# Kernel tuning notes

Hardware: AMD Instinct MI355X
Metric: run time of the kernel (lower is better)

Reference implementation:

```python
import jax, jax.numpy as jnp
import numpy as np
import math

B, S, D, H = 2, 2048, 1024, 16
HD = D // H  # head dim = 64


def setup_inputs() -> dict:
    key = jax.random.key(0)
    ks = jax.random.split(key, 8)
    scale = 1.0 / math.sqrt(D)
    return {
        "x": jax.random.normal(ks[0], (B, S, D), dtype=jnp.float32),
        "mask": jax.random.randint(ks[1], (B, S, S), 0, 2).astype(bool),
        "Wq": jax.random.normal(ks[2], (D, D), dtype=jnp.float32) * scale,
        "bq": jax.random.normal(ks[3], (D,), dtype=jnp.float32) * 0.01,
        "Wk": jax.random.normal(ks[4], (D, D), dtype=jnp.float32) * scale,
        "bk": jax.random.normal(ks[5], (D,), dtype=jnp.float32) * 0.01,
        "Wv": jax.random.normal(ks[6], (D, D), dtype=jnp.float32) * scale,
        "bv": jax.random.normal(ks[7], (D,), dtype=jnp.float32) * 0.01,
    }


def reference(x, mask, Wq, bq, Wk, bk, Wv, bv):
    # Linear projections (weights stored as [in, out])
    q = x @ Wq + bq  # [B,S,D]
    k = x @ Wk + bk
    v = x @ Wv + bv
    # split heads -> [B,H,S,HD]
    q = q.reshape(B, S, H, HD).transpose(0, 2, 1, 3)
    k = k.reshape(B, S, H, HD).transpose(0, 2, 1, 3)
    v = v.reshape(B, S, H, HD).transpose(0, 2, 1, 3)
    scores = jnp.einsum("bhqd,bhkd->bhqk", q, k) / jnp.sqrt(jnp.float32(HD))
    # Faithful to the source: masked_fill_(mask, -inf) is immediately
    # overwritten by masked_fill_(mask, 0), so masked positions end up 0
    # BEFORE the softmax (a quirk of the original module).
    scores = jnp.where(mask[:, None, :, :], 0.0, scores)
    attn = jax.nn.softmax(scores, axis=-1)  # dropout=0.0 (eval)
    out = jnp.einsum("bhqk,bhkd->bhqd", attn, v)
    return out.transpose(0, 2, 1, 3).reshape(B, S, D)
```

## Files before the change

kernel.cpp:

```cpp
#include <hip/hip_runtime.h>
#include <hip/hip_bf16.h>
#include <cstdint>
#include <cstddef>

static constexpr int B_ = 2, S_ = 2048, D_ = 1024, H_ = 16, HD_ = 64;

typedef float f32x4 __attribute__((ext_vector_type(4)));
typedef short bf16x8 __attribute__((ext_vector_type(8)));

__device__ __forceinline__ unsigned short f2bf(float f) {
    union { float f; unsigned int u; } v; v.f = f;
    unsigned int r = v.u + 0x7FFFu + ((v.u >> 16) & 1u);
    return (unsigned short)(r >> 16);
}

__device__ __forceinline__ unsigned pack2bf(float a, float b) {
#if __has_builtin(__builtin_amdgcn_cvt_pk_bf16_f32)
    auto p = __builtin_amdgcn_cvt_pk_bf16_f32(a, b);
    unsigned u; __builtin_memcpy(&u, &p, 4);
    return u;
#else
    return (unsigned)f2bf(a) | ((unsigned)f2bf(b) << 16);
#endif
}

__global__ __launch_bounds__(256)
void cast_x(const float* __restrict__ x, unsigned short* __restrict__ o) {
    size_t i = ((size_t)blockIdx.x * 256 + threadIdx.x) * 8;
    float4 a = *(const float4*)(x + i);
    float4 c = *(const float4*)(x + i + 4);
    uint4 r;
    r.x = pack2bf(a.x, a.y);
    r.y = pack2bf(a.z, a.w);
    r.z = pack2bf(c.x, c.y);
    r.w = pack2bf(c.z, c.w);
    *(uint4*)(o + i) = r;
}

__global__ __launch_bounds__(256)
void mask_pack(const int* __restrict__ m, unsigned char* __restrict__ o) {
    size_t i = ((size_t)blockIdx.x * 256 + threadIdx.x) * 16;
    uint4 r;
    unsigned w[4];
    #pragma unroll
    for (int g = 0; g < 4; ++g) {
        int4 v = *(const int4*)(m + i + g * 4);
        w[g] = (v.x ? 1u : 0u) | (v.y ? 1u << 8 : 0u) |
               (v.z ? 1u << 16 : 0u) | (v.w ? 1u << 24 : 0u);
    }
    r.x = w[0]; r.y = w[1]; r.z = w[2]; r.w = w[3];
    *(uint4*)(o + i) = r;
}

__global__ __launch_bounds__(256)
void transpose_w(const float* __restrict__ Wq, const float* __restrict__ Wk,
                 const float* __restrict__ Wv, unsigned short* __restrict__ wt) {
    const int mat = blockIdx.z;
    const float* __restrict__ W = (mat == 0) ? Wq : (mat == 1) ? Wk : Wv;
    unsigned short* __restrict__ o = wt + (size_t)mat * D_ * D_;
    const int n0 = blockIdx.x * 64, k0 = blockIdx.y * 64;
    __shared__ unsigned short Ts[64][72];
    const int t = threadIdx.x;
    {
        const int nl = t & 63, kb = t >> 6;
        #pragma unroll
        for (int i = 0; i < 16; ++i) {
            int k = kb + i * 4;
            Ts[nl][k] = f2bf(W[(size_t)(k0 + k) * D_ + n0 + nl]);
        }
    }
    __syncthreads();
    {
        const int kl = t & 63, nb = t >> 6;
        #pragma unroll
        for (int i = 0; i < 16; ++i) {
            int n = nb + i * 4;
            o[(size_t)(n0 + n) * D_ + k0 + kl] = Ts[n][kl];
        }
    }
}

__global__ __launch_bounds__(256)
void qkv_gemm(const unsigned short* __restrict__ xb, const unsigned short* __restrict__ wt,
              const float* __restrict__ bq, const float* __restrict__ bk,
              const float* __restrict__ bv,
              unsigned short* __restrict__ qo, unsigned short* __restrict__ ko,
              unsigned short* __restrict__ vto) {
    const int bx = blockIdx.x;
    const int by = blockIdx.y;
    const int mat = bx >> 3;
    const int ncol0 = (bx & 7) * 128;
    const float* __restrict__ bias = (mat == 0) ? bq : (mat == 1) ? bk : bv;
    const unsigned short* __restrict__ Wm = wt + (size_t)mat * D_ * D_;

    __shared__ unsigned short As[128][40];
    __shared__ unsigned short Bs[128][40];

    const int t = threadIdx.x;
    const int w = t >> 6, lane = t & 63;
    const int l15 = lane & 15, quad = lane >> 4;
    const int mw = (w >> 1) * 64, nw = (w & 1) * 64;
    const int rowBase = by * 128;

    f32x4 acc[4][4] = {};

    for (int kt = 0; kt < D_; kt += 32) {
        __syncthreads();
        #pragma unroll
        for (int i = 0; i < 2; ++i) {
            int c = t + i * 256;
            int r = c >> 2, q = c & 3;
            *(uint4*)&As[r][q * 8] =
                *(const uint4*)(xb + (size_t)(rowBase + r) * D_ + kt + q * 8);
            *(uint4*)&Bs[r][q * 8] =
                *(const uint4*)(Wm + (size_t)(ncol0 + r) * D_ + kt + q * 8);
        }
        __syncthreads();

        bf16x8 a[4], b[4];
        #pragma unroll
        for (int i = 0; i < 4; ++i)
            a[i] = *(const bf16x8*)&As[mw + i * 16 + l15][quad * 8];
        #pragma unroll
        for (int j = 0; j < 4; ++j)
            b[j] = *(const bf16x8*)&Bs[nw + j * 16 + l15][quad * 8];
        #pragma unroll
        for (int i = 0; i < 4; ++i)
            #pragma unroll
            for (int j = 0; j < 4; ++j)
                acc[i][j] = __builtin_amdgcn_mfma_f32_16x16x32_bf16(a[i], b[j], acc[i][j], 0, 0, 0);
    }

    if (mat < 2) {
        unsigned short* __restrict__ O = (mat == 0) ? qo : ko;
        const float osc = (mat == 0) ? 0.18033688011112443f : 1.0f;
        #pragma unroll
        for (int j = 0; j < 4; ++j) {
            const int col = ncol0 + nw + j * 16 + l15;
            const float bb = bias[col];
            #pragma unroll
            for (int i = 0; i < 4; ++i)
                #pragma unroll
                for (int r = 0; r < 4; ++r) {
                    const int m = rowBase + mw + i * 16 + quad * 4 + r;
                    O[(size_t)m * D_ + col] = f2bf((acc[i][j][r] + bb) * osc);
                }
        }
    } else {
        #pragma unroll
        for (int j = 0; j < 4; ++j) {
            const int col = ncol0 + nw + j * 16 + l15;
            const float bb = bias[col];
            const int hh = col >> 6, hd = col & 63;
            #pragma unroll
            for (int i = 0; i < 4; ++i)
                #pragma unroll
                for (int r = 0; r < 4; ++r) {
                    const int m = rowBase + mw + i * 16 + quad * 4 + r;
                    const int bg = m >> 11, s = m & 2047;
                    vto[(((size_t)bg * H_ + hh) * HD_ + hd) * S_ + s] =
                        f2bf(acc[i][j][r] + bb);
                }
        }
    }
}

__global__ __launch_bounds__(256)
void attn_mfma(const unsigned short* __restrict__ qmat,
               const unsigned short* __restrict__ kmat,
               const unsigned short* __restrict__ vtg,
               const unsigned char* __restrict__ msk, float* __restrict__ out) {
    const int h = blockIdx.x, qt = blockIdx.y, b = blockIdx.z;
    const int t = threadIdx.x, w = t >> 6, lane = t & 63;
    const int l15 = lane & 15, quad = lane >> 4;
    const int q0 = qt * 128;

    __shared__ __align__(16) unsigned short Qs[128][72];
    __shared__ __align__(16) unsigned short Ks[64][72];
    __shared__ __align__(16) unsigned short Vt[64][72];
    __shared__ __align__(16) unsigned short Ps[128][72];

    const size_t bh = (size_t)b * S_ * D_ + (size_t)h * HD_;
    const unsigned short* __restrict__ qp = qmat + bh;
    const unsigned short* __restrict__ kp = kmat + bh;
    const unsigned short* __restrict__ vp = vtg + ((size_t)b * H_ + h) * HD_ * S_;
    const unsigned char* __restrict__ mb = msk + (size_t)b * S_ * S_;

    #pragma unroll
    for (int i = 0; i < 2; ++i) {
        int c = t + i * 256;
        int r = c >> 2, cg = (c & 3) * 16;
        *(uint4*)&Qs[r][cg]     = *(const uint4*)(qp + (size_t)(q0 + r) * D_ + cg);
        *(uint4*)&Qs[r][cg + 8] = *(const uint4*)(qp + (size_t)(q0 + r) * D_ + cg + 8);
    }

    f32x4 accO[2][4] = {};
    f32x4 lsA[2] = {};
    bf16x8 ones;
    #pragma unroll
    for (int i = 0; i < 8; ++i) ones[i] = (short)0x3F80;

    const int rstage = t >> 2, cstage = (t & 3) * 16;

    for (int kt = 0; kt < S_; kt += 64) {
        __syncthreads();
        *(uint4*)&Ks[rstage][cstage]     = *(const uint4*)(kp + (size_t)(kt + rstage) * D_ + cstage);
        *(uint4*)&Ks[rstage][cstage + 8] = *(const uint4*)(kp + (size_t)(kt + rstage) * D_ + cstage + 8);
        *(uint4*)&Vt[rstage][cstage]     = *(const uint4*)(vp + (size_t)rstage * S_ + kt + cstage);
        *(uint4*)&Vt[rstage][cstage + 8] = *(const uint4*)(vp + (size_t)rstage * S_ + kt + cstage + 8);
        __syncthreads();

        f32x4 sc[4][2] = {};
        #pragma unroll
        for (int kst = 0; kst < 2; ++kst) {
            bf16x8 kfr[4], qfr[2];
            #pragma unroll
            for (int mt = 0; mt < 4; ++mt)
                kfr[mt] = *(const bf16x8*)&Ks[mt * 16 + l15][kst * 32 + quad * 8];
            #pragma unroll
            for (int nt = 0; nt < 2; ++nt)
                qfr[nt] = *(const bf16x8*)&Qs[w * 32 + nt * 16 + l15][kst * 32 + quad * 8];
            #pragma unroll
            for (int mt = 0; mt < 4; ++mt)
                #pragma unroll
                for (int nt = 0; nt < 2; ++nt)
                    sc[mt][nt] = __builtin_amdgcn_mfma_f32_16x16x32_bf16(kfr[mt], qfr[nt], sc[mt][nt], 0, 0, 0);
        }

        #pragma unroll
        for (int nt = 0; nt < 2; ++nt) {
            const int qr = w * 32 + nt * 16 + l15;
            const unsigned char* __restrict__ mrow = mb + (size_t)(q0 + qr) * S_ + kt;
            #pragma unroll
            for (int mt = 0; mt < 4; ++mt) {
                const unsigned mu = *(const unsigned*)(mrow + mt * 16 + quad * 4);
                float p[4];
                #pragma unroll
                for (int r = 0; r < 4; ++r) {
                    float e = __builtin_amdgcn_exp2f(sc[mt][nt][r]);
                    p[r] = ((mu >> (8 * r)) & 0xFFu) ? 1.0f : e;
                }
                uint2 pk;
                pk.x = pack2bf(p[0], p[1]);
                pk.y = pack2bf(p[2], p[3]);
                *(uint2*)&Ps[qr][mt * 16 + quad * 4] = pk;
            }
        }

        #pragma unroll
        for (int kst = 0; kst < 2; ++kst) {
            bf16x8 vfr[4];
            #pragma unroll
            for (int dt = 0; dt < 4; ++dt)
                vfr[dt] = *(const bf16x8*)&Vt[dt * 16 + l15][kst * 32 + quad * 8];
            #pragma unroll
            for (int mt = 0; mt < 2; ++mt) {
                bf16x8 pfr = *(const bf16x8*)&Ps[w * 32 + mt * 16 + l15][kst * 32 + quad * 8];
                #pragma unroll
                for (int dt = 0; dt < 4; ++dt)
                    accO[mt][dt] = __builtin_amdgcn_mfma_f32_16x16x32_bf16(pfr, vfr[dt], accO[mt][dt], 0, 0, 0);
                lsA[mt] = __builtin_amdgcn_mfma_f32_16x16x32_bf16(pfr, ones, lsA[mt], 0, 0, 0);
            }
        }
    }

    float* __restrict__ ob = out + ((size_t)b * S_ + q0) * D_ + (size_t)h * HD_;
    #pragma unroll
    for (int mt = 0; mt < 2; ++mt)
        #pragma unroll
        for (int r = 0; r < 4; ++r) {
            const float inv = 1.0f / lsA[mt][r];
            const int qr = w * 32 + mt * 16 + quad * 4 + r;
            #pragma unroll
            for (int dt = 0; dt < 4; ++dt)
                ob[(size_t)qr * D_ + dt * 16 + l15] = accO[mt][dt][r] * inv;
        }
}

extern "C" void kernel_launch(void* const* d_in, const int* in_sizes, int n_in,
                              void* d_out, int out_size, void* d_ws, size_t ws_size,
                              hipStream_t stream) {
    (void)in_sizes; (void)n_in; (void)out_size; (void)ws_size;
    const float* x    = (const float*)d_in[0];
    const int*   mask = (const int*)d_in[1];
    const float* Wq   = (const float*)d_in[2];
    const float* bq   = (const float*)d_in[3];
    const float* Wk   = (const float*)d_in[4];
    const float* bk   = (const float*)d_in[5];
    const float* Wv   = (const float*)d_in[6];
    const float* bv   = (const float*)d_in[7];
    float* out = (float*)d_out;

    const size_t M1 = (size_t)1024 * 1024;
    unsigned short* xb  = (unsigned short*)d_ws;
    unsigned short* wtb = xb + 4 * M1;
    unsigned short* qb  = wtb + 3 * M1;
    unsigned short* kb  = qb + 4 * M1;
    unsigned short* vtb = kb + 4 * M1;
    unsigned char*  mk  = (unsigned char*)(vtb + 4 * M1);

    cast_x<<<2048, 256, 0, stream>>>(x, xb);
    mask_pack<<<2048, 256, 0, stream>>>(mask, mk);
    transpose_w<<<dim3(16, 16, 3), 256, 0, stream>>>(Wq, Wk, Wv, wtb);
    qkv_gemm<<<dim3(24, 32), 256, 0, stream>>>(xb, wtb, bq, bk, bv, qb, kb, vtb);
    attn_mfma<<<dim3(16, 16, 2), 256, 0, stream>>>(qb, kb, vtb, mk, out);
}
```

Before: 256.6 us.

## Use direct global-to-LDS loads in QKV GEMM, keep Q in registers for attention

The QKV GEMM now stages its A and B tiles with global_load_lds, which writes straight into unpadded shared memory instead of going through registers. The V-transpose epilogue now stores four bf16 values at once instead of scattering single values. The attention kernel holds its Q fragments in registers, which removes the Qs shared buffer, and asks for 4 blocks per CU in its launch bounds. These changes aim to cut register staging, store count and LDS use so occupancy can rise, at the cost of bank conflicts in the unpadded GEMM tiles and more register pressure.

```diff
diff --git a/kernel.cpp b/kernel.cpp
--- a/kernel.cpp
+++ b/kernel.cpp
@@ -1,5 +1,4 @@
 #include <hip/hip_runtime.h>
-#include <hip/hip_bf16.h>
 #include <cstdint>
 #include <cstddef>
 
@@ -22,6 +21,12 @@
 #else
     return (unsigned)f2bf(a) | ((unsigned)f2bf(b) << 16);
 #endif
+}
+
+__device__ __forceinline__ void gload_lds16(const void* g, void* l) {
+    __builtin_amdgcn_global_load_lds(
+        (const __attribute__((address_space(1))) void*)g,
+        (__attribute__((address_space(3))) void*)l, 16, 0, 0);
 }
 
 __global__ __launch_bounds__(256)
@@ -93,8 +98,8 @@
     const float* __restrict__ bias = (mat == 0) ? bq : (mat == 1) ? bk : bv;
     const unsigned short* __restrict__ Wm = wt + (size_t)mat * D_ * D_;
 
-    __shared__ unsigned short As[128][40];
-    __shared__ unsigned short Bs[128][40];
+    __shared__ unsigned short As[128 * 32];
+    __shared__ unsigned short Bs[128 * 32];
 
     const int t = threadIdx.x;
     const int w = t >> 6, lane = t & 63;
@@ -102,28 +107,30 @@
     const int mw = (w >> 1) * 64, nw = (w & 1) * 64;
     const int rowBase = by * 128;
 
+    const int srow = lane >> 2;
+    const int scol = (lane & 3) * 8;
+
     f32x4 acc[4][4] = {};
 
     for (int kt = 0; kt < D_; kt += 32) {
         __syncthreads();
         #pragma unroll
         for (int i = 0; i < 2; ++i) {
-            int c = t + i * 256;
-            int r = c >> 2, q = c & 3;
-            *(uint4*)&As[r][q * 8] =
-                *(const uint4*)(xb + (size_t)(rowBase + r) * D_ + kt + q * 8);
-            *(uint4*)&Bs[r][q * 8] =
-                *(const uint4*)(Wm + (size_t)(ncol0 + r) * D_ + kt + q * 8);
+            const int r0 = w * 32 + i * 16;
+            gload_lds16(xb + (size_t)(rowBase + r0 + srow) * D_ + kt + scol,
+                        &As[r0 * 32]);
+            gload_lds16(Wm + (size_t)(ncol0 + r0 + srow) * D_ + kt + scol,
+                        &Bs[r0 * 32]);
         }
         __syncthreads();
 
         bf16x8 a[4], b[4];
         #pragma unroll
         for (int i = 0; i < 4; ++i)
-            a[i] = *(const bf16x8*)&As[mw + i * 16 + l15][quad * 8];
+            a[i] = *(const bf16x8*)&As[(mw + i * 16 + l15) * 32 + quad * 8];
         #pragma unroll
         for (int j = 0; j < 4; ++j)
-            b[j] = *(const bf16x8*)&Bs[nw + j * 16 + l15][quad * 8];
+            b[j] = *(const bf16x8*)&Bs[(nw + j * 16 + l15) * 32 + quad * 8];
         #pragma unroll
         for (int i = 0; i < 4; ++i)
             #pragma unroll
@@ -153,19 +160,21 @@
             const float bb = bias[col];
             const int hh = col >> 6, hd = col & 63;
             #pragma unroll
-            for (int i = 0; i < 4; ++i)
-                #pragma unroll
-                for (int r = 0; r < 4; ++r) {
-                    const int m = rowBase + mw + i * 16 + quad * 4 + r;
-                    const int bg = m >> 11, s = m & 2047;
-                    vto[(((size_t)bg * H_ + hh) * HD_ + hd) * S_ + s] =
-                        f2bf(acc[i][j][r] + bb);
-                }
-        }
-    }
-}
-
-__global__ __launch_bounds__(256)
+            for (int i = 0; i < 4; ++i) {
+                const int m0 = rowBase + mw + i * 16 + quad * 4;
+                const int bg = m0 >> 11, s0 = m0 & 2047;
+                ushort4 pk;
+                pk.x = f2bf(acc[i][j][0] + bb);
+                pk.y = f2bf(acc[i][j][1] + bb);
+                pk.z = f2bf(acc[i][j][2] + bb);
+                pk.w = f2bf(acc[i][j][3] + bb);
+                *(ushort4*)&vto[(((size_t)bg * H_ + hh) * HD_ + hd) * S_ + s0] = pk;
+            }
+        }
+    }
+}
+
+__global__ __launch_bounds__(256, 4)
 void attn_mfma(const unsigned short* __restrict__ qmat,
                const unsigned short* __restrict__ kmat,
                const unsigned short* __restrict__ vtg,
@@ -175,7 +184,6 @@
     const int l15 = lane & 15, quad = lane >> 4;
     const int q0 = qt * 128;
 
-    __shared__ __align__(16) unsigned short Qs[128][72];
     __shared__ __align__(16) unsigned short Ks[64][72];
     __shared__ __align__(16) unsigned short Vt[64][72];
     __shared__ __align__(16) unsigned short Ps[128][72];
@@ -186,13 +194,13 @@
     const unsigned short* __restrict__ vp = vtg + ((size_t)b * H_ + h) * HD_ * S_;
     const unsigned char* __restrict__ mb = msk + (size_t)b * S_ * S_;
 
+    bf16x8 qfr[2][2];
     #pragma unroll
-    for (int i = 0; i < 2; ++i) {
-        int c = t + i * 256;
-        int r = c >> 2, cg = (c & 3) * 16;
-        *(uint4*)&Qs[r][cg]     = *(const uint4*)(qp + (size_t)(q0 + r) * D_ + cg);
-        *(uint4*)&Qs[r][cg + 8] = *(const uint4*)(qp + (size_t)(q0 + r) * D_ + cg + 8);
-    }
+    for (int nt = 0; nt < 2; ++nt)
+        #pragma unroll
+        for (int kst = 0; kst < 2; ++kst)
+            qfr[nt][kst] = *(const bf16x8*)(qp +
+                (size_t)(q0 + w * 32 + nt * 16 + l15) * D_ + kst * 32 + quad * 8);
 
     f32x4 accO[2][4] = {};
     f32x4 lsA[2] = {};
@@ -213,18 +221,15 @@
         f32x4 sc[4][2] = {};
         #pragma unroll
         for (int kst = 0; kst < 2; ++kst) {
-            bf16x8 kfr[4], qfr[2];
+            bf16x8 kfr[4];
             #pragma unroll
             for (int mt = 0; mt < 4; ++mt)
                 kfr[mt] = *(const bf16x8*)&Ks[mt * 16 + l15][kst * 32 + quad * 8];
-            #pragma unroll
-            for (int nt = 0; nt < 2; ++nt)
-                qfr[nt] = *(const bf16x8*)&Qs[w * 32 + nt * 16 + l15][kst * 32 + quad * 8];
             #pragma unroll
             for (int mt = 0; mt < 4; ++mt)
                 #pragma unroll
                 for (int nt = 0; nt < 2; ++nt)
-                    sc[mt][nt] = __builtin_amdgcn_mfma_f32_16x16x32_bf16(kfr[mt], qfr[nt], sc[mt][nt], 0, 0, 0);
+                    sc[mt][nt] = __builtin_amdgcn_mfma_f32_16x16x32_bf16(kfr[mt], qfr[nt][kst], sc[mt][nt], 0, 0, 0);
         }
 
         #pragma unroll
```

New measurement: 252.5 us. Within noise of the previous version (-1.6%).
